# Optimization experiments

Hardware: AMD Instinct MI355X
Metric: run time of the kernel (lower is better)

## Reference

```python
import jax, jax.numpy as jnp
import numpy as np

CHANNEL = 256
MEM_SIZE = 684
POS_NUM = 128
NEG_NUM = 512
TEMP = 1.0
CLASS_NUM = 60
BANK_ROWS = MEM_SIZE * CLASS_NUM  # 41040
BATCH = 512


def setup_inputs() -> dict:
    key = jax.random.key(0)
    k1, k2, k3, k4 = jax.random.split(key, 4)
    f = jax.random.normal(k1, (BATCH, CHANNEL), dtype=jnp.float32)
    f_normed = f / jnp.linalg.norm(f, axis=-1, keepdims=True)
    label = jax.random.randint(k2, (BATCH,), 0, CLASS_NUM, dtype=jnp.int32)
    bank = jax.random.normal(k3, (BANK_ROWS, CHANNEL), dtype=jnp.float32)
    bank = bank / jnp.linalg.norm(bank, axis=-1, keepdims=True)
    bank_flag = jnp.ones((BANK_ROWS,), dtype=jnp.float32)  # warmed-up bank
    rand_neg = jax.random.uniform(k4, (BATCH, BANK_ROWS), dtype=jnp.float32)
    # exact torch roundrobin enqueue logic (sequential over the batch)
    rr = np.zeros(CLASS_NUM, dtype=np.int64)
    idxs = []
    for i in np.asarray(label).tolist():
        rr[i] = rr[i] + 1 if rr[i] < CLASS_NUM - 1 else 0
        idxs.append(int(rr[i]) + i * MEM_SIZE)
    enqueue_idx = jnp.asarray(idxs, dtype=jnp.int32)
    return {"f_normed": f_normed, "label": label, "enqueue_idx": enqueue_idx,
            "bank": bank, "bank_flag": bank_flag, "rand_neg": rand_neg}


def reference(f_normed, label, enqueue_idx, bank, bank_flag, rand_neg):
    N = f_normed.shape[0]
    # enqueue (detached write, as in torch: Bank[indies] = f_normed.detach())
    bank = bank.at[enqueue_idx].set(jax.lax.stop_gradient(f_normed))
    flag = bank_flag.at[enqueue_idx].set(1.0)
    # all_pairs: [N, M]
    all_pairs = jnp.einsum('nc,mc->nm', f_normed, bank)
    bank_label = jnp.tile(jnp.arange(CLASS_NUM), MEM_SIZE)  # arange(C).repeat(mem)
    eq = label[:, None] == bank_label[None, :]
    valid = flag > 0
    pos_mask = eq & valid
    neg_mask = (~eq) & valid
    # hard positives: smallest POS_NUM positive similarities per row
    pos_hard = jnp.sort(jnp.where(pos_mask, all_pairs, jnp.inf), axis=-1)[:, :POS_NUM]
    # hard negatives: largest NEG_NUM negative similarities per row
    neg_hard, _ = jax.lax.top_k(jnp.where(neg_mask, all_pairs, -jnp.inf), NEG_NUM)
    # random negatives: uniform sample without replacement via noise argsort
    r = jnp.where(neg_mask, rand_neg, jnp.inf)
    rand_idx = jnp.argsort(r, axis=-1)[:, :NEG_NUM]
    neg_rand = jnp.take_along_axis(all_pairs, rand_idx, axis=-1)
    # combined logits: [N, 2*POS_NUM, 1+NEG_NUM]
    pos = pos_hard[:, :, None]
    h2h = jnp.concatenate([pos, jnp.broadcast_to(neg_hard[:, None, :], (N, POS_NUM, NEG_NUM))], axis=-1)
    h2r = jnp.concatenate([pos, jnp.broadcast_to(neg_rand[:, None, :], (N, POS_NUM, NEG_NUM))], axis=-1)
    combined = jnp.concatenate([h2h, h2r], axis=1).reshape(-1, 1 + NEG_NUM)
    # cross entropy with target class 0 for every row
    loss = -jnp.mean(jax.nn.log_softmax(combined / TEMP, axis=-1)[:, 0])
    return loss
```

## Files before the change

### kernel.cpp

```cpp
#include <hip/hip_runtime.h>

#define CH    256
#define MEM   684
#define POSN  128
#define NEGN  512
#define CLS   60
#define ROWS  41040
#define BATCHN 512

typedef unsigned int u32;
typedef unsigned short u16;
typedef unsigned long long u64;

typedef __attribute__((ext_vector_type(8))) short bf16x8;
typedef __attribute__((ext_vector_type(4))) float f32x4;

__device__ __forceinline__ float b2f(u16 u) { return __uint_as_float(((u32)u) << 16); }
__device__ __forceinline__ u16 f2b(float x) {
  u32 u = __float_as_uint(x);
  u32 r = ((u >> 16) & 1u) + 0x7FFFu;
  return (u16)((u + r) >> 16);
}
__device__ __forceinline__ u32 umin2(u32 a, u32 b) { return a < b ? a : b; }

#if defined(__has_builtin)
#if __has_builtin(__builtin_amdgcn_global_load_lds)
#define HAVE_GLL 1
#endif
#endif

__device__ __forceinline__ void stage16(const u16* g, u16* l) {
#ifdef HAVE_GLL
  __builtin_amdgcn_global_load_lds((const __attribute__((address_space(1))) void*)g,
                                   (__attribute__((address_space(3))) void*)l, 16, 0, 0);
#else
  *(uint4*)l = *(const uint4*)g;
#endif
}

__global__ __launch_bounds__(256) void k_convert(const float* __restrict__ bank,
                                                 u16* __restrict__ bankB) {
  size_t i = (size_t)(blockIdx.x * 256 + threadIdx.x) * 8;
  float4 a = *(const float4*)(bank + i);
  float4 b = *(const float4*)(bank + i + 4);
  uint4 o;
  o.x = (u32)f2b(a.x) | ((u32)f2b(a.y) << 16);
  o.y = (u32)f2b(a.z) | ((u32)f2b(a.w) << 16);
  o.z = (u32)f2b(b.x) | ((u32)f2b(b.y) << 16);
  o.w = (u32)f2b(b.z) | ((u32)f2b(b.w) << 16);
  *(uint4*)(bankB + i) = o;
}

__global__ __launch_bounds__(256) void k_scatter(const float* __restrict__ f,
                                                 const int* __restrict__ enq,
                                                 u16* __restrict__ fB,
                                                 u16* __restrict__ bankB) {
  int n = blockIdx.x, t = threadIdx.x;
  u16 v = f2b(f[n * CH + t]);
  fB[n * CH + t] = v;
  int row = enq[n];
  bankB[(size_t)row * CH + t] = v;
}

__global__ __launch_bounds__(256) void k_gemm(const u16* __restrict__ fB,
                                              const u16* __restrict__ bankB,
                                              u16* __restrict__ Cb) {
  __shared__ __align__(16) u16 As[128 * 32];
  __shared__ __align__(16) u16 Bs[128 * 32];
  const int tid = threadIdx.x;
  const int wave = tid >> 6, lane = tid & 63;
  const int bm = blockIdx.x * 128;
  const int bn = blockIdx.y * 128;
  const int wm = (wave & 1) * 64, wn = (wave >> 1) * 64;
  const int m_in = lane & 15;
  const int ks = (lane >> 4) * 8;

  f32x4 acc[4][4] = {};

  for (int k0 = 0; k0 < CH; k0 += 32) {
    __syncthreads();
#pragma unroll
    for (int i = 0; i < 2; i++) {
      int u = tid + 256 * i;
      int row = u >> 2;
      int kk = (u & 3) * 8;
      stage16(fB + (size_t)(bm + row) * CH + k0 + kk, As + u * 8);
      int rb = bn + row;
      if (rb >= ROWS) rb = bn;
      stage16(bankB + (size_t)rb * CH + k0 + kk, Bs + u * 8);
    }
    __syncthreads();

    bf16x8 af[4], bf[4];
#pragma unroll
    for (int t4 = 0; t4 < 4; t4++) {
      af[t4] = *(const bf16x8*)(As + (wm + t4 * 16 + m_in) * 32 + ks);
      bf[t4] = *(const bf16x8*)(Bs + (wn + t4 * 16 + m_in) * 32 + ks);
    }
#pragma unroll
    for (int mi = 0; mi < 4; mi++)
#pragma unroll
      for (int ni = 0; ni < 4; ni++)
        acc[mi][ni] = __builtin_amdgcn_mfma_f32_16x16x32_bf16(af[mi], bf[ni], acc[mi][ni], 0, 0, 0);
  }

  const int rr = (lane >> 4) * 4;
  const int cc = lane & 15;
#pragma unroll
  for (int mi = 0; mi < 4; mi++) {
#pragma unroll
    for (int ni = 0; ni < 4; ni++) {
      int ncol = bn + wn + ni * 16 + cc;
      if (ncol < ROWS) {
        size_t base = (size_t)(bm + wm + mi * 16 + rr) * ROWS + ncol;
#pragma unroll
        for (int q = 0; q < 4; q++) Cb[base + (size_t)q * ROWS] = f2b(acc[mi][ni][q]);
      }
    }
  }
}

__device__ __forceinline__ u32 wscan_incl(u32 v) {
  int lane = (int)(threadIdx.x & 63);
#pragma unroll
  for (int off = 1; off < 64; off <<= 1) {
    u32 t = __shfl_up(v, off, 64);
    if (lane >= off) v += t;
  }
  return v;
}

__device__ __forceinline__ u32 wave_multi_append(u32* cnt, u32 nc) {
  u32 inc = wscan_incl(nc);
  u32 base = 0;
  if ((threadIdx.x & 63) == 63) base = atomicAdd(cnt, inc);
  base = __shfl(base, 63, 64);
  return base + inc - nc;
}

__device__ __forceinline__ u32 scan1024(u32 v, u32* tmp, int tid) {
  u32 inc = wscan_incl(v);
  int wid = tid >> 6;
  if ((tid & 63) == 63) tmp[wid] = inc;
  __syncthreads();
  if (tid < 64) {
    u32 t = (tid < 16) ? tmp[tid] : 0u;
    u32 ti = wscan_incl(t);
    if (tid < 16) tmp[tid] = ti - t;
  }
  __syncthreads();
  u32 r = inc + tmp[wid];
  __syncthreads();
  return r;
}

__device__ __forceinline__ float redsum1024(float v, float* tmp, int tid) {
#pragma unroll
  for (int off = 32; off > 0; off >>= 1) v += __shfl_xor(v, off, 64);
  int wid = tid >> 6;
  if ((tid & 63) == 0) tmp[wid] = v;
  __syncthreads();
  if (tid == 0) {
    float t = 0.f;
#pragma unroll
    for (int i = 0; i < 16; i++) t += tmp[i];
    tmp[0] = t;
  }
  __syncthreads();
  float r = tmp[0];
  __syncthreads();
  return r;
}

__device__ __forceinline__ int binof(float v, float lo, float scale) {
  int b = (int)((v - lo) * scale);
  return b < 0 ? 0 : (b > 2047 ? 2047 : b);
}

#define VITER 5
#define VTAIL 80
#define VTAILBASE 40960
#define CAPC 3072
#define CAPR 1536

__global__ __launch_bounds__(1024, 8) void k_select(const u16* __restrict__ Cb,
                                                    const float* __restrict__ rnd,
                                                    const int* __restrict__ label,
                                                    float* __restrict__ partial) {
  const int n = blockIdx.x;
  const int tid = threadIdx.x;
  const u16* crow = Cb + (size_t)n * ROWS;
  const float* rrow = rnd + (size_t)n * ROWS;
  const int lab = label[n];

  __shared__ __align__(16) char smem[56448];
  u32* histc = (u32*)(smem);
  u32* histr = (u32*)(smem + 8192);
  float* clist = (float*)(smem + 16384);
  float* rl_rv = (float*)(smem + 28672);
  float* rl_cv = (float*)(smem + 34816);
  u32* rl_mi = (u32*)(smem + 40960);
  u32* stmp = (u32*)(smem + 47104);
  float* fred = (float*)(smem + 47104);
  float* cb_c = (float*)(smem + 51200);
  float* rb_r = (float*)(smem + 53248);
  float* rb_c = (float*)(smem + 54272);
  u32* rb_m = (u32*)(smem + 55296);
  u32* ctl = (u32*)(smem + 56320);
  float* bc_f = (float*)(ctl + 8);

  const int rv0 = (tid * 8) % 60;

  float T1 = 0.09375f;
  float T0 = 0.03125f;
  u32 F = 0, G = 0;
  float sc_c, sc_r;

  for (int attempt = 0;; attempt++) {
    for (int i = tid; i < 2048; i += 1024) { histc[i] = 0; histr[i] = 0; }
    if (tid == 0) { ctl[0] = 0; ctl[1] = 0; }
    __syncthreads();
    sc_c = 2048.0f / (1.0625f - T1);
    sc_r = 2048.0f / T0;
    int rb = rv0;
    for (int it = 0; it < VITER; it++) {
      int m8 = (it * 1024 + tid) * 8;
      uint4 cr = *(const uint4*)(crow + m8);
      float4 ra = *(const float4*)(rrow + m8);
      float4 rb4 = *(const float4*)(rrow + m8 + 4);
      u32 cw[4] = {cr.x, cr.y, cr.z, cr.w};
      float rs[8] = {ra.x, ra.y, ra.z, ra.w, rb4.x, rb4.y, rb4.z, rb4.w};
      float cv_[8];
      u32 nc = 0, nr = 0;
      int r = rb;
#pragma unroll
      for (int j = 0; j < 8; j++) {
        bool isneg = (r != lab);
        float c = b2f((u16)(cw[j >> 1] >> ((j & 1) * 16)));
        cv_[j] = c;
        nc += (isneg && c > T1) ? 1u : 0u;
        nr += (isneg && rs[j] < T0) ? 1u : 0u;
        r++;
        if (r == 60) r = 0;
      }
      u32 s1 = wave_multi_append(&ctl[0], nc);
      u32 s2 = wave_multi_append(&ctl[1], nr);
      r = rb;
#pragma unroll
      for (int j = 0; j < 8; j++) {
        bool isneg = (r != lab);
        float c = cv_[j];
        if (isneg && c > T1) {
          if (s1 < CAPC) clist[s1] = c;
          atomicAdd(&histc[binof(c, T1, sc_c)], 1u);
          s1++;
        }
        float rv = rs[j];
        if (isneg && rv < T0) {
          if (s2 < CAPR) { rl_rv[s2] = rv; rl_cv[s2] = c; rl_mi[s2] = (u32)(m8 + j); }
          atomicAdd(&histr[binof(rv, 0.0f, sc_r)], 1u);
          s2++;
        }
        r++;
        if (r == 60) r = 0;
      }
      rb += 32;
      if (rb >= 60) rb -= 60;
    }
    {
      const bool act = tid < VTAIL;
      float c = 0.f, rv = 1.f;
      bool pc = false, pr = false;
      int m = VTAILBASE + tid;
      if (act) {
        int r = 40 + tid;
        if (r >= 60) r -= 60;
        bool isneg = (r != lab);
        c = b2f(crow[m]);
        rv = rrow[m];
        pc = isneg && (c > T1);
        pr = isneg && (rv < T0);
      }
      u32 s1 = wave_multi_append(&ctl[0], pc ? 1u : 0u);
      u32 s2 = wave_multi_append(&ctl[1], pr ? 1u : 0u);
      if (pc) {
        if (s1 < CAPC) clist[s1] = c;
        atomicAdd(&histc[binof(c, T1, sc_c)], 1u);
      }
      if (pr) {
        if (s2 < CAPR) { rl_rv[s2] = rv; rl_cv[s2] = c; rl_mi[s2] = (u32)m; }
        atomicAdd(&histr[binof(rv, 0.0f, sc_r)], 1u);
      }
    }
    __syncthreads();
    F = ctl[0];
    G = ctl[1];
    __syncthreads();
    if (F >= NEGN && G >= NEGN) break;
    if (F < NEGN) T1 = -1.1f;
    if (G < NEGN) T0 = 1.1f;
  }
  const bool listc_ok = (F <= CAPC);
  const bool listr_ok = (G <= CAPR);

  if (tid == 0) { ctl[2] = 0; ctl[3] = 0; ctl[4] = 0; ctl[5] = 0; ctl[6] = 0; ctl[7] = 0; }
  u32 fsum = histc[tid * 2] + histc[tid * 2 + 1];
  u32 finc = scan1024(fsum, stmp, tid);
  u32 fexc = finc - fsum;
  u32 tcpos = F - NEGN + 1;
  if (fexc < tcpos && tcpos <= finc) {
    u32 run = fexc;
#pragma unroll
    for (int i = 0; i < 2; i++) {
      u32 h = histc[tid * 2 + i];
      if (run + h >= tcpos) { ctl[4] = (u32)(tid * 2 + i); ctl[5] = F - (run + h); break; }
      run += h;
    }
  }
  __syncthreads();
  const u32 b_c = ctl[4], cnt_gt = ctl[5];

  u32 gsum = histr[tid * 2] + histr[tid * 2 + 1];
  u32 ginc = scan1024(gsum, stmp, tid);
  u32 gexc = ginc - gsum;
  if (gexc < NEGN && NEGN <= ginc) {
    u32 run = gexc;
#pragma unroll
    for (int i = 0; i < 2; i++) {
      u32 h = histr[tid * 2 + i];
      if (run + h >= NEGN) { ctl[6] = (u32)(tid * 2 + i); ctl[7] = run; break; }
      run += h;
    }
  }
  __syncthreads();
  const u32 b_r = ctl[6], cnt_lt = ctl[7];
  const u32 need_c = NEGN - cnt_gt;
  const u32 need_r = NEGN - cnt_lt;

  float sH = 0.f, sR = 0.f;
  if (listc_ok) {
    for (u32 i = tid; i < F; i += 1024) {
      float c = clist[i];
      u32 b = (u32)binof(c, T1, sc_c);
      if (b > b_c) sH += expf(c);
      else if (b == b_c) {
        u32 id = atomicAdd(&ctl[2], 1u);
        if (id < 512) cb_c[id] = c;
      }
    }
  }
  if (listr_ok) {
    for (u32 i = tid; i < G; i += 1024) {
      float rv = rl_rv[i];
      u32 b = (u32)binof(rv, 0.0f, sc_r);
      if (b < b_r) sR += expf(rl_cv[i]);
      else if (b == b_r) {
        u32 id = atomicAdd(&ctl[3], 1u);
        if (id < 256) { rb_r[id] = rv; rb_c[id] = rl_cv[i]; rb_m[id] = rl_mi[i]; }
      }
    }
  }
  if (!listc_ok || !listr_ok) {
    for (int m = tid; m < ROWS; m += 1024) {
      int r = m % 60;
      if (r == lab) continue;
      float c = b2f(crow[m]);
      if (!listc_ok && c > T1) {
        u32 b = (u32)binof(c, T1, sc_c);
        if (b > b_c) sH += expf(c);
        else if (b == b_c) {
          u32 id = atomicAdd(&ctl[2], 1u);
          if (id < 512) cb_c[id] = c;
        }
      }
      if (!listr_ok) {
        float rv = rrow[m];
        if (rv < T0) {
          u32 b = (u32)binof(rv, 0.0f, sc_r);
          if (b < b_r) sR += expf(c);
          else if (b == b_r) {
            u32 id = atomicAdd(&ctl[3], 1u);
            if (id < 256) { rb_r[id] = rv; rb_c[id] = c; rb_m[id] = (u32)m; }
          }
        }
      }
    }
  }
  __syncthreads();
  float SHsum = redsum1024(sH, fred, tid);
  float SRsum = redsum1024(sR, fred, tid);

  if (tid == 0) {
    float addH = 0.f;
    u32 Lc = umin2(ctl[2], 512u);
    u32 kc = umin2(need_c, Lc);
    for (u32 k = 0; k < kc; k++) {
      int best = 0;
      float bv = -3.0e38f;
      for (u32 i = 0; i < Lc; i++)
        if (cb_c[i] > bv) { bv = cb_c[i]; best = (int)i; }
      cb_c[best] = -3.0e38f;
      addH += expf(bv);
    }
    u32 Lr = umin2(ctl[3], 256u);
    for (u32 i = 1; i < Lr; i++) {
      float rv = rb_r[i]; u32 mm = rb_m[i]; float cv = rb_c[i];
      int j = (int)i - 1;
      while (j >= 0 && (rb_r[j] > rv || (rb_r[j] == rv && rb_m[j] > mm))) {
        rb_r[j + 1] = rb_r[j]; rb_m[j + 1] = rb_m[j]; rb_c[j + 1] = rb_c[j];
        j--;
      }
      rb_r[j + 1] = rv; rb_m[j + 1] = mm; rb_c[j + 1] = cv;
    }
    float addR = 0.f;
    u32 kr = umin2(need_r, Lr);
    for (u32 i = 0; i < kr; i++) addR += expf(rb_c[i]);
    bc_f[0] = addH;
    bc_f[1] = addR;
  }
  __syncthreads();
  const float S_H = SHsum + bc_f[0];
  const float S_R = SRsum + bc_f[1];
  __syncthreads();

  float pval = 0.f;
  int pbin = 0;
  const bool hasp = tid < MEM;
  const float PLO = -1.03125f;
  const float PSC = 2048.0f / 2.09375f;
  if (hasp) {
    pval = b2f(crow[lab + CLS * tid]);
    pbin = binof(pval, PLO, PSC);
  }
  for (int i = tid; i < 2048; i += 1024) histc[i] = 0;
  if (tid == 0) { ctl[2] = 0; ctl[4] = 0; ctl[5] = 0; }
  __syncthreads();
  if (hasp) atomicAdd(&histc[pbin], 1u);
  __syncthreads();
  u32 hsum = histc[tid * 2] + histc[tid * 2 + 1];
  u32 hinc = scan1024(hsum, stmp, tid);
  u32 hexc = hinc - hsum;
  if (hexc < POSN && POSN <= hinc) {
    u32 run = hexc;
#pragma unroll
    for (int i = 0; i < 2; i++) {
      u32 h = histc[tid * 2 + i];
      if (run + h >= POSN) { ctl[4] = (u32)(tid * 2 + i); ctl[5] = run; break; }
      run += h;
    }
  }
  __syncthreads();
  const u32 b_p = ctl[4], cnt_below = ctl[5];
  const u32 need_p = POSN - cnt_below;
  if (hasp && (u32)pbin == b_p) {
    u32 id = atomicAdd(&ctl[2], 1u);
    if (id < 512) cb_c[id] = pval;
  }
  float term = 0.f;
  if (hasp && (u32)pbin < b_p) {
    float e = expf(pval);
    term = (pval - logf(e + S_H)) + (pval - logf(e + S_R));
  }
  __syncthreads();
  if (tid == 0) {
    u32 L = umin2(ctl[2], 512u);
    u32 kp = umin2(need_p, L);
    float add = 0.f;
    for (u32 k = 0; k < kp; k++) {
      int best = 0;
      float bv = 3.0e38f;
      for (u32 i = 0; i < L; i++)
        if (cb_c[i] < bv) { bv = cb_c[i]; best = (int)i; }
      cb_c[best] = 3.0e38f;
      float e = expf(bv);
      add += (bv - logf(e + S_H)) + (bv - logf(e + S_R));
    }
    bc_f[0] = add;
  }
  __syncthreads();
  float tot = redsum1024(term, fred, tid);
  if (tid == 0) partial[n] = tot + bc_f[0];
}

__global__ __launch_bounds__(256) void k_final(const float* __restrict__ partial,
                                               float* __restrict__ out) {
  __shared__ float fred[256];
  int tid = threadIdx.x;
  float v = partial[tid] + partial[tid + 256];
  fred[tid] = v;
  __syncthreads();
  for (int off = 128; off > 0; off >>= 1) {
    if (tid < off) fred[tid] += fred[tid + off];
    __syncthreads();
  }
  if (tid == 0) out[0] = -fred[0] / (float)(BATCHN * 2 * POSN);
}

extern "C" void kernel_launch(void* const* d_in, const int* in_sizes, int n_in,
                              void* d_out, int out_size, void* d_ws, size_t ws_size,
                              hipStream_t stream) {
  const float* f = (const float*)d_in[0];
  const int* label = (const int*)d_in[1];
  const int* enq = (const int*)d_in[2];
  const float* bank = (const float*)d_in[3];
  const float* rnd = (const float*)d_in[5];
  float* out = (float*)d_out;

  char* ws = (char*)d_ws;
  u16* bankB = (u16*)ws;
  u16* fB = (u16*)(ws + 21012480);
  u16* Cb = (u16*)(ws + 21012480 + 262144);
  float* partial = (float*)(ws + 21012480 + 262144 + 42024960);

  k_convert<<<dim3(5130), dim3(256), 0, stream>>>(bank, bankB);
  k_scatter<<<dim3(BATCHN), dim3(256), 0, stream>>>(f, enq, fB, bankB);
  k_gemm<<<dim3(4, 321), dim3(256), 0, stream>>>(fB, bankB, Cb);
  k_select<<<dim3(BATCHN), dim3(1024), 0, stream>>>(Cb, rnd, label, partial);
  k_final<<<dim3(1), dim3(256), 0, stream>>>(partial, out);
}
```

Before: 237.2 us.

## Keep similarity row in registers, remap GEMM blocks per XCD, vectorize C stores

k_select now loads each thread's bf16 similarity chunk into registers once and reuses it for both the histogram pass and the threshold-sum pass. This removes the shared-memory candidate list and its wave-scan append, and the total count F is taken from the histogram scan instead. The GEMM becomes a 1D grid with an XCD-aware block remap so that blocks sharing bank columns land on the same XCD. Its MFMA operands are swapped so each lane holds four consecutive columns, which are written as one packed 64-bit store. These changes cut LDS use, atomics and strided global stores, at the cost of more registers per thread in k_select.

```diff
diff --git a/kernel.cpp b/kernel.cpp
--- a/kernel.cpp
+++ b/kernel.cpp
@@ -69,8 +69,14 @@
   __shared__ __align__(16) u16 Bs[128 * 32];
   const int tid = threadIdx.x;
   const int wave = tid >> 6, lane = tid & 63;
-  const int bm = blockIdx.x * 128;
-  const int bn = blockIdx.y * 128;
+
+  const u32 id = blockIdx.x;
+  const u32 q = 160u, r4 = 4u;
+  const u32 xcd = id & 7u, jj = id >> 3;
+  const u32 wg = (xcd < r4 ? xcd * (q + 1u) : r4 * (q + 1u) + (xcd - r4) * q) + jj;
+  const int bm = (int)(wg & 3u) * 128;
+  const int bn = (int)(wg >> 2) * 128;
+
   const int wm = (wave & 1) * 64, wn = (wave >> 1) * 64;
   const int m_in = lane & 15;
   const int ks = (lane >> 4) * 8;
@@ -101,20 +107,21 @@
     for (int mi = 0; mi < 4; mi++)
 #pragma unroll
       for (int ni = 0; ni < 4; ni++)
-        acc[mi][ni] = __builtin_amdgcn_mfma_f32_16x16x32_bf16(af[mi], bf[ni], acc[mi][ni], 0, 0, 0);
-  }
-
+        acc[mi][ni] = __builtin_amdgcn_mfma_f32_16x16x32_bf16(bf[ni], af[mi], acc[mi][ni], 0, 0, 0);
+  }
+
+  const int cc = lane & 15;
   const int rr = (lane >> 4) * 4;
-  const int cc = lane & 15;
 #pragma unroll
   for (int mi = 0; mi < 4; mi++) {
+    const int row = bm + wm + mi * 16 + cc;
 #pragma unroll
     for (int ni = 0; ni < 4; ni++) {
-      int ncol = bn + wn + ni * 16 + cc;
-      if (ncol < ROWS) {
-        size_t base = (size_t)(bm + wm + mi * 16 + rr) * ROWS + ncol;
-#pragma unroll
-        for (int q = 0; q < 4; q++) Cb[base + (size_t)q * ROWS] = f2b(acc[mi][ni][q]);
+      const int n0 = bn + wn + ni * 16 + rr;
+      if (n0 < ROWS) {
+        u64 pk = (u64)f2b(acc[mi][ni][0]) | ((u64)f2b(acc[mi][ni][1]) << 16) |
+                 ((u64)f2b(acc[mi][ni][2]) << 32) | ((u64)f2b(acc[mi][ni][3]) << 48);
+        *(u64*)(Cb + (size_t)row * ROWS + n0) = pk;
       }
     }
   }
@@ -128,14 +135,6 @@
     if (lane >= off) v += t;
   }
   return v;
-}
-
-__device__ __forceinline__ u32 wave_multi_append(u32* cnt, u32 nc) {
-  u32 inc = wscan_incl(nc);
-  u32 base = 0;
-  if ((threadIdx.x & 63) == 63) base = atomicAdd(cnt, inc);
-  base = __shfl(base, 63, 64);
-  return base + inc - nc;
 }
 
 __device__ __forceinline__ u32 scan1024(u32 v, u32* tmp, int tid) {
@@ -180,7 +179,6 @@
 #define VITER 5
 #define VTAIL 80
 #define VTAILBASE 40960
-#define CAPC 3072
 #define CAPR 1536
 
 __global__ __launch_bounds__(1024, 8) void k_select(const u16* __restrict__ Cb,
@@ -193,120 +191,112 @@
   const float* rrow = rnd + (size_t)n * ROWS;
   const int lab = label[n];
 
-  __shared__ __align__(16) char smem[56448];
+  __shared__ __align__(16) char smem[44160];
   u32* histc = (u32*)(smem);
   u32* histr = (u32*)(smem + 8192);
-  float* clist = (float*)(smem + 16384);
-  float* rl_rv = (float*)(smem + 28672);
-  float* rl_cv = (float*)(smem + 34816);
-  u32* rl_mi = (u32*)(smem + 40960);
-  u32* stmp = (u32*)(smem + 47104);
-  float* fred = (float*)(smem + 47104);
-  float* cb_c = (float*)(smem + 51200);
-  float* rb_r = (float*)(smem + 53248);
-  float* rb_c = (float*)(smem + 54272);
-  u32* rb_m = (u32*)(smem + 55296);
-  u32* ctl = (u32*)(smem + 56320);
+  float* rl_rv = (float*)(smem + 16384);
+  float* rl_cv = (float*)(smem + 22528);
+  u32* rl_mi = (u32*)(smem + 28672);
+  u32* stmp = (u32*)(smem + 34816);
+  float* fred = (float*)(smem + 34816);
+  float* cb_c = (float*)(smem + 38912);
+  float* rb_r = (float*)(smem + 40960);
+  float* rb_c = (float*)(smem + 41984);
+  u32* rb_m = (u32*)(smem + 43008);
+  u32* ctl = (u32*)(smem + 44032);
   float* bc_f = (float*)(ctl + 8);
 
   const int rv0 = (tid * 8) % 60;
+
+  uint4 creg[VITER];
+#pragma unroll
+  for (int it = 0; it < VITER; it++)
+    creg[it] = *(const uint4*)(crow + (it * 1024 + tid) * 8);
+  const bool act = tid < VTAIL;
+  float c_tail = 0.f;
+  bool tail_neg = false;
+  if (act) {
+    c_tail = b2f(crow[VTAILBASE + tid]);
+    int r = 40 + tid;
+    if (r >= 60) r -= 60;
+    tail_neg = (r != lab);
+  }
 
   float T1 = 0.09375f;
   float T0 = 0.03125f;
   u32 F = 0, G = 0;
   float sc_c, sc_r;
+  u32 fsum = 0, finc = 0, fexc = 0;
 
   for (int attempt = 0;; attempt++) {
     for (int i = tid; i < 2048; i += 1024) { histc[i] = 0; histr[i] = 0; }
-    if (tid == 0) { ctl[0] = 0; ctl[1] = 0; }
+    if (tid == 0) ctl[1] = 0;
     __syncthreads();
     sc_c = 2048.0f / (1.0625f - T1);
     sc_r = 2048.0f / T0;
     int rb = rv0;
+#pragma unroll
     for (int it = 0; it < VITER; it++) {
       int m8 = (it * 1024 + tid) * 8;
-      uint4 cr = *(const uint4*)(crow + m8);
+      uint4 cr = creg[it];
       float4 ra = *(const float4*)(rrow + m8);
       float4 rb4 = *(const float4*)(rrow + m8 + 4);
       u32 cw[4] = {cr.x, cr.y, cr.z, cr.w};
       float rs[8] = {ra.x, ra.y, ra.z, ra.w, rb4.x, rb4.y, rb4.z, rb4.w};
-      float cv_[8];
-      u32 nc = 0, nr = 0;
+      bool pr[8];
+      u32 nr = 0;
       int r = rb;
 #pragma unroll
       for (int j = 0; j < 8; j++) {
         bool isneg = (r != lab);
         float c = b2f((u16)(cw[j >> 1] >> ((j & 1) * 16)));
-        cv_[j] = c;
-        nc += (isneg && c > T1) ? 1u : 0u;
-        nr += (isneg && rs[j] < T0) ? 1u : 0u;
+        if (isneg && c > T1) atomicAdd(&histc[binof(c, T1, sc_c)], 1u);
+        pr[j] = isneg && (rs[j] < T0);
+        nr += pr[j] ? 1u : 0u;
         r++;
         if (r == 60) r = 0;
       }
-      u32 s1 = wave_multi_append(&ctl[0], nc);
-      u32 s2 = wave_multi_append(&ctl[1], nr);
-      r = rb;
+      u32 s2 = 0;
+      if (nr) s2 = atomicAdd(&ctl[1], nr);
 #pragma unroll
       for (int j = 0; j < 8; j++) {
-        bool isneg = (r != lab);
-        float c = cv_[j];
-        if (isneg && c > T1) {
-          if (s1 < CAPC) clist[s1] = c;
-          atomicAdd(&histc[binof(c, T1, sc_c)], 1u);
-          s1++;
-        }
-        float rv = rs[j];
-        if (isneg && rv < T0) {
+        if (pr[j]) {
+          float rv = rs[j];
+          float c = b2f((u16)(cw[j >> 1] >> ((j & 1) * 16)));
           if (s2 < CAPR) { rl_rv[s2] = rv; rl_cv[s2] = c; rl_mi[s2] = (u32)(m8 + j); }
           atomicAdd(&histr[binof(rv, 0.0f, sc_r)], 1u);
           s2++;
         }
-        r++;
-        if (r == 60) r = 0;
       }
       rb += 32;
       if (rb >= 60) rb -= 60;
     }
-    {
-      const bool act = tid < VTAIL;
-      float c = 0.f, rv = 1.f;
-      bool pc = false, pr = false;
-      int m = VTAILBASE + tid;
-      if (act) {
-        int r = 40 + tid;
-        if (r >= 60) r -= 60;
-        bool isneg = (r != lab);
-        c = b2f(crow[m]);
-        rv = rrow[m];
-        pc = isneg && (c > T1);
-        pr = isneg && (rv < T0);
-      }
-      u32 s1 = wave_multi_append(&ctl[0], pc ? 1u : 0u);
-      u32 s2 = wave_multi_append(&ctl[1], pr ? 1u : 0u);
-      if (pc) {
-        if (s1 < CAPC) clist[s1] = c;
-        atomicAdd(&histc[binof(c, T1, sc_c)], 1u);
-      }
-      if (pr) {
-        if (s2 < CAPR) { rl_rv[s2] = rv; rl_cv[s2] = c; rl_mi[s2] = (u32)m; }
+    if (act) {
+      if (tail_neg && c_tail > T1) atomicAdd(&histc[binof(c_tail, T1, sc_c)], 1u);
+      float rv = rrow[VTAILBASE + tid];
+      if (tail_neg && rv < T0) {
+        u32 s2 = atomicAdd(&ctl[1], 1u);
+        if (s2 < CAPR) { rl_rv[s2] = rv; rl_cv[s2] = c_tail; rl_mi[s2] = (u32)(VTAILBASE + tid); }
         atomicAdd(&histr[binof(rv, 0.0f, sc_r)], 1u);
       }
     }
     __syncthreads();
+    G = ctl[1];
+    fsum = histc[tid * 2] + histc[tid * 2 + 1];
+    finc = scan1024(fsum, stmp, tid);
+    fexc = finc - fsum;
+    if (tid == 1023) ctl[0] = finc;
+    __syncthreads();
     F = ctl[0];
-    G = ctl[1];
-    __syncthreads();
     if (F >= NEGN && G >= NEGN) break;
     if (F < NEGN) T1 = -1.1f;
     if (G < NEGN) T0 = 1.1f;
-  }
-  const bool listc_ok = (F <= CAPC);
+    __syncthreads();
+  }
   const bool listr_ok = (G <= CAPR);
 
   if (tid == 0) { ctl[2] = 0; ctl[3] = 0; ctl[4] = 0; ctl[5] = 0; ctl[6] = 0; ctl[7] = 0; }
-  u32 fsum = histc[tid * 2] + histc[tid * 2 + 1];
-  u32 finc = scan1024(fsum, stmp, tid);
-  u32 fexc = finc - fsum;
+  __syncthreads();
   u32 tcpos = F - NEGN + 1;
   if (fexc < tcpos && tcpos <= finc) {
     u32 run = fexc;
@@ -317,9 +307,6 @@
       run += h;
     }
   }
-  __syncthreads();
-  const u32 b_c = ctl[4], cnt_gt = ctl[5];
-
   u32 gsum = histr[tid * 2] + histr[tid * 2 + 1];
   u32 ginc = scan1024(gsum, stmp, tid);
   u32 gexc = ginc - gsum;
@@ -333,19 +320,43 @@
     }
   }
   __syncthreads();
+  const u32 b_c = ctl[4], cnt_gt = ctl[5];
   const u32 b_r = ctl[6], cnt_lt = ctl[7];
   const u32 need_c = NEGN - cnt_gt;
   const u32 need_r = NEGN - cnt_lt;
 
   float sH = 0.f, sR = 0.f;
-  if (listc_ok) {
-    for (u32 i = tid; i < F; i += 1024) {
-      float c = clist[i];
-      u32 b = (u32)binof(c, T1, sc_c);
-      if (b > b_c) sH += expf(c);
+  {
+    int rb = rv0;
+#pragma unroll
+    for (int it = 0; it < VITER; it++) {
+      uint4 cr = creg[it];
+      u32 cw[4] = {cr.x, cr.y, cr.z, cr.w};
+      int r = rb;
+#pragma unroll
+      for (int j = 0; j < 8; j++) {
+        bool isneg = (r != lab);
+        float c = b2f((u16)(cw[j >> 1] >> ((j & 1) * 16)));
+        if (isneg && c > T1) {
+          u32 b = (u32)binof(c, T1, sc_c);
+          if (b > b_c) sH += expf(c);
+          else if (b == b_c) {
+            u32 id = atomicAdd(&ctl[2], 1u);
+            if (id < 512) cb_c[id] = c;
+          }
+        }
+        r++;
+        if (r == 60) r = 0;
+      }
+      rb += 32;
+      if (rb >= 60) rb -= 60;
+    }
+    if (act && tail_neg && c_tail > T1) {
+      u32 b = (u32)binof(c_tail, T1, sc_c);
+      if (b > b_c) sH += expf(c_tail);
       else if (b == b_c) {
         u32 id = atomicAdd(&ctl[2], 1u);
-        if (id < 512) cb_c[id] = c;
+        if (id < 512) cb_c[id] = c_tail;
       }
     }
   }
@@ -359,29 +370,18 @@
         if (id < 256) { rb_r[id] = rv; rb_c[id] = rl_cv[i]; rb_m[id] = rl_mi[i]; }
       }
     }
-  }
-  if (!listc_ok || !listr_ok) {
+  } else {
     for (int m = tid; m < ROWS; m += 1024) {
       int r = m % 60;
       if (r == lab) continue;
-      float c = b2f(crow[m]);
-      if (!listc_ok && c > T1) {
-        u32 b = (u32)binof(c, T1, sc_c);
-        if (b > b_c) sH += expf(c);
-        else if (b == b_c) {
-          u32 id = atomicAdd(&ctl[2], 1u);
-          if (id < 512) cb_c[id] = c;
-        }
-      }
-      if (!listr_ok) {
-        float rv = rrow[m];
-        if (rv < T0) {
-          u32 b = (u32)binof(rv, 0.0f, sc_r);
-          if (b < b_r) sR += expf(c);
-          else if (b == b_r) {
-            u32 id = atomicAdd(&ctl[3], 1u);
-            if (id < 256) { rb_r[id] = rv; rb_c[id] = c; rb_m[id] = (u32)m; }
-          }
+      float rv = rrow[m];
+      if (rv < T0) {
+        float c = b2f(crow[m]);
+        u32 b = (u32)binof(rv, 0.0f, sc_r);
+        if (b < b_r) sR += expf(c);
+        else if (b == b_r) {
+          u32 id = atomicAdd(&ctl[3], 1u);
+          if (id < 256) { rb_r[id] = rv; rb_c[id] = c; rb_m[id] = (u32)m; }
         }
       }
     }
@@ -514,7 +514,7 @@
 
   k_convert<<<dim3(5130), dim3(256), 0, stream>>>(bank, bankB);
   k_scatter<<<dim3(BATCHN), dim3(256), 0, stream>>>(f, enq, fB, bankB);
-  k_gemm<<<dim3(4, 321), dim3(256), 0, stream>>>(fB, bankB, Cb);
+  k_gemm<<<dim3(1284), dim3(256), 0, stream>>>(fB, bankB, Cb);
   k_select<<<dim3(BATCHN), dim3(1024), 0, stream>>>(Cb, rnd, label, partial);
   k_final<<<dim3(1), dim3(256), 0, stream>>>(partial, out);
 }
```

Result: slower. 290.6 us (+22.5%).

## Remap GEMM blocks per XCD, vectorize C stores, simplify select append path

Applied to the files above, without the earlier changes.

The GEMM moves to a 1D grid and remaps block IDs so that consecutive tiles land on the same XCD, which should improve L2 reuse of the bank tiles. It also swaps the MFMA operands so each lane holds four consecutive output columns, and packs them into one 64-bit store instead of four strided 16-bit stores. In the select kernel, the wave-level scan plus a single atomic per wave is replaced by per-thread LDS atomics, and the main loop is unrolled. One barrier is removed by merging the two histogram-threshold reads. The per-thread atomics increase LDS atomic contention and change the order of list entries.

```diff
diff --git a/kernel.cpp b/kernel.cpp
--- a/kernel.cpp
+++ b/kernel.cpp
@@ -69,8 +69,14 @@
   __shared__ __align__(16) u16 Bs[128 * 32];
   const int tid = threadIdx.x;
   const int wave = tid >> 6, lane = tid & 63;
-  const int bm = blockIdx.x * 128;
-  const int bn = blockIdx.y * 128;
+
+  const u32 id = blockIdx.x;
+  const u32 q = 160u, r4 = 4u;
+  const u32 xcd = id & 7u, jj = id >> 3;
+  const u32 wg = (xcd < r4 ? xcd * (q + 1u) : r4 * (q + 1u) + (xcd - r4) * q) + jj;
+  const int bm = (int)(wg & 3u) * 128;
+  const int bn = (int)(wg >> 2) * 128;
+
   const int wm = (wave & 1) * 64, wn = (wave >> 1) * 64;
   const int m_in = lane & 15;
   const int ks = (lane >> 4) * 8;
@@ -101,20 +107,21 @@
     for (int mi = 0; mi < 4; mi++)
 #pragma unroll
       for (int ni = 0; ni < 4; ni++)
-        acc[mi][ni] = __builtin_amdgcn_mfma_f32_16x16x32_bf16(af[mi], bf[ni], acc[mi][ni], 0, 0, 0);
-  }
-
+        acc[mi][ni] = __builtin_amdgcn_mfma_f32_16x16x32_bf16(bf[ni], af[mi], acc[mi][ni], 0, 0, 0);
+  }
+
+  const int cc = lane & 15;
   const int rr = (lane >> 4) * 4;
-  const int cc = lane & 15;
 #pragma unroll
   for (int mi = 0; mi < 4; mi++) {
+    const int row = bm + wm + mi * 16 + cc;
 #pragma unroll
     for (int ni = 0; ni < 4; ni++) {
-      int ncol = bn + wn + ni * 16 + cc;
-      if (ncol < ROWS) {
-        size_t base = (size_t)(bm + wm + mi * 16 + rr) * ROWS + ncol;
-#pragma unroll
-        for (int q = 0; q < 4; q++) Cb[base + (size_t)q * ROWS] = f2b(acc[mi][ni][q]);
+      const int n0 = bn + wn + ni * 16 + rr;
+      if (n0 < ROWS) {
+        u64 pk = (u64)f2b(acc[mi][ni][0]) | ((u64)f2b(acc[mi][ni][1]) << 16) |
+                 ((u64)f2b(acc[mi][ni][2]) << 32) | ((u64)f2b(acc[mi][ni][3]) << 48);
+        *(u64*)(Cb + (size_t)row * ROWS + n0) = pk;
       }
     }
   }
@@ -128,14 +135,6 @@
     if (lane >= off) v += t;
   }
   return v;
-}
-
-__device__ __forceinline__ u32 wave_multi_append(u32* cnt, u32 nc) {
-  u32 inc = wscan_incl(nc);
-  u32 base = 0;
-  if ((threadIdx.x & 63) == 63) base = atomicAdd(cnt, inc);
-  base = __shfl(base, 63, 64);
-  return base + inc - nc;
 }
 
 __device__ __forceinline__ u32 scan1024(u32 v, u32* tmp, int tid) {
@@ -223,6 +222,7 @@
     sc_c = 2048.0f / (1.0625f - T1);
     sc_r = 2048.0f / T0;
     int rb = rv0;
+#pragma unroll
     for (int it = 0; it < VITER; it++) {
       int m8 = (it * 1024 + tid) * 8;
       uint4 cr = *(const uint4*)(crow + m8);
@@ -230,64 +230,55 @@
       float4 rb4 = *(const float4*)(rrow + m8 + 4);
       u32 cw[4] = {cr.x, cr.y, cr.z, cr.w};
       float rs[8] = {ra.x, ra.y, ra.z, ra.w, rb4.x, rb4.y, rb4.z, rb4.w};
-      float cv_[8];
+      float cv[8];
+      bool pc[8], pr[8];
       u32 nc = 0, nr = 0;
       int r = rb;
 #pragma unroll
       for (int j = 0; j < 8; j++) {
         bool isneg = (r != lab);
         float c = b2f((u16)(cw[j >> 1] >> ((j & 1) * 16)));
-        cv_[j] = c;
-        nc += (isneg && c > T1) ? 1u : 0u;
-        nr += (isneg && rs[j] < T0) ? 1u : 0u;
+        cv[j] = c;
+        pc[j] = isneg && (c > T1);
+        pr[j] = isneg && (rs[j] < T0);
+        nc += pc[j] ? 1u : 0u;
+        nr += pr[j] ? 1u : 0u;
         r++;
         if (r == 60) r = 0;
       }
-      u32 s1 = wave_multi_append(&ctl[0], nc);
-      u32 s2 = wave_multi_append(&ctl[1], nr);
-      r = rb;
+      u32 s1 = 0, s2 = 0;
+      if (nc) s1 = atomicAdd(&ctl[0], nc);
+      if (nr) s2 = atomicAdd(&ctl[1], nr);
 #pragma unroll
       for (int j = 0; j < 8; j++) {
-        bool isneg = (r != lab);
-        float c = cv_[j];
-        if (isneg && c > T1) {
-          if (s1 < CAPC) clist[s1] = c;
-          atomicAdd(&histc[binof(c, T1, sc_c)], 1u);
+        if (pc[j]) {
+          if (s1 < CAPC) clist[s1] = cv[j];
+          atomicAdd(&histc[binof(cv[j], T1, sc_c)], 1u);
           s1++;
         }
-        float rv = rs[j];
-        if (isneg && rv < T0) {
-          if (s2 < CAPR) { rl_rv[s2] = rv; rl_cv[s2] = c; rl_mi[s2] = (u32)(m8 + j); }
-          atomicAdd(&histr[binof(rv, 0.0f, sc_r)], 1u);
+        if (pr[j]) {
+          if (s2 < CAPR) { rl_rv[s2] = rs[j]; rl_cv[s2] = cv[j]; rl_mi[s2] = (u32)(m8 + j); }
+          atomicAdd(&histr[binof(rs[j], 0.0f, sc_r)], 1u);
           s2++;
         }
-        r++;
-        if (r == 60) r = 0;
       }
       rb += 32;
       if (rb >= 60) rb -= 60;
     }
-    {
-      const bool act = tid < VTAIL;
-      float c = 0.f, rv = 1.f;
-      bool pc = false, pr = false;
+    if (tid < VTAIL) {
       int m = VTAILBASE + tid;
-      if (act) {
-        int r = 40 + tid;
-        if (r >= 60) r -= 60;
-        bool isneg = (r != lab);
-        c = b2f(crow[m]);
-        rv = rrow[m];
-        pc = isneg && (c > T1);
-        pr = isneg && (rv < T0);
-      }
-      u32 s1 = wave_multi_append(&ctl[0], pc ? 1u : 0u);
-      u32 s2 = wave_multi_append(&ctl[1], pr ? 1u : 0u);
-      if (pc) {
+      int r = 40 + tid;
+      if (r >= 60) r -= 60;
+      bool isneg = (r != lab);
+      float c = b2f(crow[m]);
+      if (isneg && c > T1) {
+        u32 s1 = atomicAdd(&ctl[0], 1u);
         if (s1 < CAPC) clist[s1] = c;
         atomicAdd(&histc[binof(c, T1, sc_c)], 1u);
       }
-      if (pr) {
+      float rv = rrow[m];
+      if (isneg && rv < T0) {
+        u32 s2 = atomicAdd(&ctl[1], 1u);
         if (s2 < CAPR) { rl_rv[s2] = rv; rl_cv[s2] = c; rl_mi[s2] = (u32)m; }
         atomicAdd(&histr[binof(rv, 0.0f, sc_r)], 1u);
       }
@@ -317,9 +308,6 @@
       run += h;
     }
   }
-  __syncthreads();
-  const u32 b_c = ctl[4], cnt_gt = ctl[5];
-
   u32 gsum = histr[tid * 2] + histr[tid * 2 + 1];
   u32 ginc = scan1024(gsum, stmp, tid);
   u32 gexc = ginc - gsum;
@@ -333,6 +321,7 @@
     }
   }
   __syncthreads();
+  const u32 b_c = ctl[4], cnt_gt = ctl[5];
   const u32 b_r = ctl[6], cnt_lt = ctl[7];
   const u32 need_c = NEGN - cnt_gt;
   const u32 need_r = NEGN - cnt_lt;
@@ -514,7 +503,7 @@
 
   k_convert<<<dim3(5130), dim3(256), 0, stream>>>(bank, bankB);
   k_scatter<<<dim3(BATCHN), dim3(256), 0, stream>>>(f, enq, fB, bankB);
-  k_gemm<<<dim3(4, 321), dim3(256), 0, stream>>>(fB, bankB, Cb);
+  k_gemm<<<dim3(1284), dim3(256), 0, stream>>>(fB, bankB, Cb);
   k_select<<<dim3(BATCHN), dim3(1024), 0, stream>>>(Cb, rnd, label, partial);
   k_final<<<dim3(1), dim3(256), 0, stream>>>(partial, out);
 }
```

Result: slower. 284.8 us (+20.1%).
